# Kernel tuning notes

Measured on AMD Instinct MI355X. Metric: run time of the kernel, lower is better.

Reference implementation:

```python
import jax, jax.numpy as jnp
import numpy as np

HUGE = 1e31  # ops.HUGE_INT
EPS = 1e-20

NUM_ENT, NUM_REL = 100000, 400
ENT_D, REL_D, HIST_D = 256, 256, 512
ACT_D = ENT_D + REL_D          # 512
IN_D = ENT_D + HIST_D + REL_D  # 1024
B, A = 512, 256


def setup_inputs() -> dict:
    key = jax.random.key(0)
    ks = jax.random.split(key, 10)
    s = 0.02
    return {
        "current_entity": jax.random.randint(ks[0], (B,), 0, NUM_ENT),
        "query_relation": jax.random.randint(ks[1], (B,), 0, NUM_REL),
        "encoded_history": jax.random.normal(ks[2], (B, HIST_D), jnp.float32),
        "r_space": jax.random.randint(ks[3], (B, A), 0, NUM_REL),
        "e_space": jax.random.randint(ks[4], (B, A), 0, NUM_ENT),
        "action_mask": jax.random.randint(ks[5], (B, A), 0, 2).astype(jnp.int32),
        "entity_emb": jax.random.normal(ks[6], (NUM_ENT, ENT_D), jnp.float32) * s,
        "relation_emb": jax.random.normal(ks[7], (NUM_REL, REL_D), jnp.float32) * s,
        "W1": jax.random.normal(ks[8], (IN_D, ACT_D), jnp.float32) * s,
        "b1": jnp.zeros((ACT_D,), jnp.float32),
        "W2": jax.random.normal(ks[9], (ACT_D, ACT_D), jnp.float32) * s,
        "b2": jnp.zeros((ACT_D,), jnp.float32),
    }


def reference(current_entity, query_relation, encoded_history, r_space, e_space,
              action_mask, entity_emb, relation_emb, W1, b1, W2, b2):
    # encode_history: [E(cur) | lstm hidden | R(query)] -> [B, IN_D]
    X = jnp.concatenate([entity_emb[current_entity], encoded_history,
                         relation_emb[query_relation]], axis=-1)
    # policy MLP (dropout = identity in eval)
    X2 = jax.nn.relu(X @ W1 + b1) @ W2 + b2          # [B, ACT_D]
    # per-action embeddings: concat(rel, ent) -> [B, A, ACT_D]
    A_emb = jnp.concatenate([relation_emb[r_space], entity_emb[e_space]], axis=-1)
    mask = action_mask.astype(X2.dtype)
    scores = jnp.einsum('bad,bd->ba', A_emb, X2) - (1.0 - mask) * HUGE
    action_dist = jax.nn.softmax(scores, axis=-1)    # [B, A]
    entropy = -jnp.sum(action_dist * jnp.log(action_dist + EPS), axis=-1)  # [B]
    return action_dist, entropy
```

## Files before the change

kernel.cpp:

```cpp
#include <hip/hip_runtime.h>
#include <hip/hip_bf16.h>

#define ENT_D 256
#define REL_D 256
#define HIST_D 512
#define ACT_DD 512
#define IN_DD 1024
#define BB 512
#define AA 256

typedef short bf16x8 __attribute__((ext_vector_type(8)));
typedef float floatx4 __attribute__((ext_vector_type(4)));

__device__ __forceinline__ unsigned short f2bf(float f) {
    unsigned u = __builtin_bit_cast(unsigned, f);
    return (unsigned short)((u + 0x7fffu + ((u >> 16) & 1u)) >> 16);
}


__global__ __launch_bounds__(256) void pack_kernel(
    const int* __restrict__ cur, const int* __restrict__ qrel,
    const float* __restrict__ hist,
    const float* __restrict__ ent_emb, const float* __restrict__ rel_emb,
    const float* __restrict__ W1, const float* __restrict__ W2,
    unsigned short* __restrict__ W1p, unsigned short* __restrict__ W2p,
    unsigned short* __restrict__ Xp)
{
    const int wid  = blockIdx.x * 4 + (threadIdx.x >> 6);
    const int lane = threadIdx.x & 63;
    const int l15  = lane & 15;
    const int quad = lane >> 4;
    unsigned short v[8];

    if (wid < 1024) {
        const int t = wid, nt = t >> 5, kt = t & 31;
        const int n = nt * 16 + l15, k0 = kt * 32 + quad * 8;
#pragma unroll
        for (int j = 0; j < 8; ++j) v[j] = f2bf(W1[(size_t)(k0 + j) * ACT_DD + n]);
        *(bf16x8*)(W1p + ((size_t)t * 64 + lane) * 8) = *(bf16x8*)v;
    } else if (wid < 1536) {
        const int t = wid - 1024, nt = t >> 4, kt = t & 15;
        const int n = nt * 16 + l15, k0 = kt * 32 + quad * 8;
#pragma unroll
        for (int j = 0; j < 8; ++j) v[j] = f2bf(W2[(size_t)(k0 + j) * ACT_DD + n]);
        *(bf16x8*)(W2p + ((size_t)t * 64 + lane) * 8) = *(bf16x8*)v;
    } else {
        const int t = wid - 1536, mt = t >> 5, kt = t & 31;
        const int m = mt * 16 + l15, k0 = kt * 32 + quad * 8;
        const float* src;
        if (k0 < ENT_D)            src = ent_emb + (size_t)cur[m] * ENT_D + k0;
        else if (k0 < ENT_D + HIST_D) src = hist + (size_t)m * HIST_D + (k0 - ENT_D);
        else                       src = rel_emb + (size_t)qrel[m] * REL_D + (k0 - ENT_D - HIST_D);
        float4 a = *(const float4*)src, b = *(const float4*)(src + 4);
        v[0]=f2bf(a.x); v[1]=f2bf(a.y); v[2]=f2bf(a.z); v[3]=f2bf(a.w);
        v[4]=f2bf(b.x); v[5]=f2bf(b.y); v[6]=f2bf(b.z); v[7]=f2bf(b.w);
        *(bf16x8*)(Xp + ((size_t)t * 64 + lane) * 8) = *(bf16x8*)v;
    }
}

__global__ __launch_bounds__(256) void gemm1_kernel(
    const unsigned short* __restrict__ Xp, const unsigned short* __restrict__ W1p,
    const float* __restrict__ b1, unsigned short* __restrict__ Hp)
{
    __shared__ unsigned short sH[1024];
    const int mt = blockIdx.x, wave = threadIdx.x >> 6, lane = threadIdx.x & 63;
    const int nt = blockIdx.y * 4 + wave;

    const bf16x8* Av = (const bf16x8*)Xp  + (size_t)mt * 32 * 64 + lane;
    const bf16x8* Bv = (const bf16x8*)W1p + (size_t)nt * 32 * 64 + lane;
    floatx4 acc = {0.f, 0.f, 0.f, 0.f};
#pragma unroll 8
    for (int kt = 0; kt < 32; ++kt)
        acc = __builtin_amdgcn_mfma_f32_16x16x32_bf16(Av[kt * 64], Bv[kt * 64], acc, 0, 0, 0);

    const int col  = nt * 16 + (lane & 15);
    const float bj = b1[col];
    const int n_loc = wave * 16 + (lane & 15);
    const int tile_loc = n_loc >> 5, quad2 = (n_loc & 31) >> 3, j2 = n_loc & 7;
#pragma unroll
    for (int reg = 0; reg < 4; ++reg) {
        const int row = (lane >> 4) * 4 + reg;
        const float h = fmaxf(acc[reg] + bj, 0.f);
        sH[tile_loc * 512 + (row + 16 * quad2) * 8 + j2] = f2bf(h);
    }
    __syncthreads();
    const int h = threadIdx.x * 4;
    const int tl = h >> 9, rest = h & 511;
    const size_t dst = ((size_t)(mt * 16 + blockIdx.y * 2 + tl) * 512 + rest);
    *(uint2*)(Hp + dst) = *(const uint2*)(sH + h);
}

__global__ __launch_bounds__(256) void gemm2_kernel(
    const unsigned short* __restrict__ Hp, const unsigned short* __restrict__ W2p,
    const float* __restrict__ b2, float* __restrict__ X2)
{
    const int mt = blockIdx.x, wave = threadIdx.x >> 6, lane = threadIdx.x & 63;
    const int nt = blockIdx.y * 4 + wave;

    const bf16x8* Av = (const bf16x8*)Hp  + (size_t)mt * 16 * 64 + lane;
    const bf16x8* Bv = (const bf16x8*)W2p + (size_t)nt * 16 * 64 + lane;
    floatx4 acc = {0.f, 0.f, 0.f, 0.f};
#pragma unroll
    for (int kt = 0; kt < 16; ++kt)
        acc = __builtin_amdgcn_mfma_f32_16x16x32_bf16(Av[kt * 64], Bv[kt * 64], acc, 0, 0, 0);

    const int col = nt * 16 + (lane & 15);
    const float bj = b2[col];
#pragma unroll
    for (int reg = 0; reg < 4; ++reg) {
        const int m = mt * 16 + (lane >> 4) * 4 + reg;
        X2[(size_t)m * ACT_DD + col] = acc[reg] + bj;
    }
}

__global__ __launch_bounds__(512) void score_softmax_kernel(
    const float* __restrict__ X2,
    const int* __restrict__ r_space, const int* __restrict__ e_space,
    const int* __restrict__ amask,
    const float* __restrict__ ent_emb, const float* __restrict__ rel_emb,
    float* __restrict__ dist, float* __restrict__ ent_out)
{
    __shared__ __align__(16) float x2s[ACT_DD];
    __shared__ float sc[AA];
    __shared__ int   list[AA];
    __shared__ int   wcnt[4];
    __shared__ int   n_u_s;
    __shared__ float red[8];

    const int b = blockIdx.x, tid = threadIdx.x;
    const int wave = tid >> 6, lane = tid & 63;

    x2s[tid] = X2[(size_t)b * ACT_DD + tid];

    int m = 0;
    unsigned long long bal = 0;
    int pre = 0;
    if (tid < AA) {
        m = amask[b * AA + tid];
        sc[tid] = 0.0f;
    }
    if (wave < 4) {
        bal = __ballot(m != 0);
        pre = __popcll(bal & ((1ull << lane) - 1ull));
        if (lane == 0) wcnt[wave] = __popcll(bal);
    }
    __syncthreads();

    if (wave < 4) {
        int off = 0;
#pragma unroll
        for (int w = 0; w < 4; ++w) if (w < wave) off += wcnt[w];
        if (m != 0) list[off + pre] = tid;
        if (tid == 0) n_u_s = wcnt[0] + wcnt[1] + wcnt[2] + wcnt[3];
    }
    __syncthreads();

    const int n_u = n_u_s;
    const int padded = (n_u + 63) & ~63;
    if (tid < padded - n_u) list[n_u + tid] = list[0];
    __syncthreads();

    const float4 xr = ((const float4*)&x2s[0])[lane];
    const float4 xe = ((const float4*)&x2s[REL_D])[lane];

    for (int base = wave * 8; base < padded; base += 64) {
        int ai[8], ir[8], ie[8];
#pragma unroll
        for (int i = 0; i < 8; ++i) ai[i] = list[base + i];
#pragma unroll
        for (int i = 0; i < 8; ++i) {
            ir[i] = r_space[b * AA + ai[i]];
            ie[i] = e_space[b * AA + ai[i]];
        }
        float4 r4[8], e4[8];
#pragma unroll
        for (int i = 0; i < 8; ++i)
            r4[i] = ((const float4*)(rel_emb + (size_t)ir[i] * REL_D))[lane];
#pragma unroll
        for (int i = 0; i < 8; ++i)
            e4[i] = ((const float4*)(ent_emb + (size_t)ie[i] * ENT_D))[lane];

        __builtin_amdgcn_sched_barrier(0);

        float p[8];
#pragma unroll
        for (int i = 0; i < 8; ++i)
            p[i] = r4[i].x * xr.x + r4[i].y * xr.y + r4[i].z * xr.z + r4[i].w * xr.w
                 + e4[i].x * xe.x + e4[i].y * xe.y + e4[i].z * xe.z + e4[i].w * xe.w;
#pragma unroll
        for (int off = 32; off > 0; off >>= 1) {
#pragma unroll
            for (int i = 0; i < 8; ++i) p[i] += __shfl_xor(p[i], off, 64);
        }
        if (lane == 0) {
#pragma unroll
            for (int i = 0; i < 8; ++i) sc[ai[i]] = p[i];
        }
    }
    __syncthreads();

    float s = -3.0e38f;
    if (tid < AA) s = (m != 0) ? sc[tid] : (sc[tid] - 1e31f);
    float v = s;
#pragma unroll
    for (int off = 32; off > 0; off >>= 1) v = fmaxf(v, __shfl_xor(v, off, 64));
    if (lane == 0) red[wave] = v;
    __syncthreads();
    float mx = red[0];
#pragma unroll
    for (int w = 1; w < 8; ++w) mx = fmaxf(mx, red[w]);
    __syncthreads();

    const float e = (tid < AA) ? __expf(s - mx) : 0.0f;
    v = e;
#pragma unroll
    for (int off = 32; off > 0; off >>= 1) v += __shfl_xor(v, off, 64);
    if (lane == 0) red[wave] = v;
    __syncthreads();
    float sum = red[0];
#pragma unroll
    for (int w = 1; w < 8; ++w) sum += red[w];
    __syncthreads();

    const float p = e / sum;
    if (tid < AA) dist[(size_t)b * AA + tid] = p;

    v = (tid < AA) ? p * __logf(p + 1e-20f) : 0.0f;
#pragma unroll
    for (int off = 32; off > 0; off >>= 1) v += __shfl_xor(v, off, 64);
    if (lane == 0) red[wave] = v;
    __syncthreads();
    if (tid == 0) {
        float t = red[0];
#pragma unroll
        for (int w = 1; w < 8; ++w) t += red[w];
        ent_out[b] = -t;
    }
}

extern "C" void kernel_launch(void* const* d_in, const int* in_sizes, int n_in,
                              void* d_out, int out_size, void* d_ws, size_t ws_size,
                              hipStream_t stream) {
    const int*   cur      = (const int*)d_in[0];
    const int*   qrel     = (const int*)d_in[1];
    const float* hist     = (const float*)d_in[2];
    const int*   r_space  = (const int*)d_in[3];
    const int*   e_space  = (const int*)d_in[4];
    const int*   amask    = (const int*)d_in[5];
    const float* ent_emb  = (const float*)d_in[6];
    const float* rel_emb  = (const float*)d_in[7];
    const float* W1       = (const float*)d_in[8];
    const float* b1       = (const float*)d_in[9];
    const float* W2       = (const float*)d_in[10];
    const float* b2       = (const float*)d_in[11];

    float* dist    = (float*)d_out;
    float* entropy = dist + (size_t)BB * AA;

    char* w = (char*)d_ws;
    unsigned short* W1p = (unsigned short*)(w);
    unsigned short* W2p = (unsigned short*)(w + (1u << 20));
    unsigned short* Xp  = (unsigned short*)(w + (3u << 19));
    unsigned short* Hp  = (unsigned short*)(w + (5u << 19));
    float*          X2  = (float*)(w + (6u << 19));

    pack_kernel<<<640, 256, 0, stream>>>(cur, qrel, hist, ent_emb, rel_emb, W1, W2, W1p, W2p, Xp);
    gemm1_kernel<<<dim3(32, 8), 256, 0, stream>>>(Xp, W1p, b1, Hp);
    gemm2_kernel<<<dim3(32, 8), 256, 0, stream>>>(Hp, W2p, b2, X2);
    score_softmax_kernel<<<512, 512, 0, stream>>>(X2, r_space, e_space, amask,
                                                  ent_emb, rel_emb, dist, entropy);
}
```

Measured before the change: 180.1 us.

## Fuse bf16 packing of weights and inputs into the GEMM kernels

```diff
diff --git a/kernel.cpp b/kernel.cpp
--- a/kernel.cpp
+++ b/kernel.cpp
@@ -18,98 +18,97 @@
 }
 
 
-__global__ __launch_bounds__(256) void pack_kernel(
+__global__ __launch_bounds__(256) void gemm1_kernel(
     const int* __restrict__ cur, const int* __restrict__ qrel,
     const float* __restrict__ hist,
     const float* __restrict__ ent_emb, const float* __restrict__ rel_emb,
-    const float* __restrict__ W1, const float* __restrict__ W2,
-    unsigned short* __restrict__ W1p, unsigned short* __restrict__ W2p,
-    unsigned short* __restrict__ Xp)
-{
-    const int wid  = blockIdx.x * 4 + (threadIdx.x >> 6);
-    const int lane = threadIdx.x & 63;
-    const int l15  = lane & 15;
-    const int quad = lane >> 4;
-    unsigned short v[8];
-
-    if (wid < 1024) {
-        const int t = wid, nt = t >> 5, kt = t & 31;
-        const int n = nt * 16 + l15, k0 = kt * 32 + quad * 8;
-#pragma unroll
-        for (int j = 0; j < 8; ++j) v[j] = f2bf(W1[(size_t)(k0 + j) * ACT_DD + n]);
-        *(bf16x8*)(W1p + ((size_t)t * 64 + lane) * 8) = *(bf16x8*)v;
-    } else if (wid < 1536) {
-        const int t = wid - 1024, nt = t >> 4, kt = t & 15;
-        const int n = nt * 16 + l15, k0 = kt * 32 + quad * 8;
-#pragma unroll
-        for (int j = 0; j < 8; ++j) v[j] = f2bf(W2[(size_t)(k0 + j) * ACT_DD + n]);
-        *(bf16x8*)(W2p + ((size_t)t * 64 + lane) * 8) = *(bf16x8*)v;
-    } else {
-        const int t = wid - 1536, mt = t >> 5, kt = t & 31;
-        const int m = mt * 16 + l15, k0 = kt * 32 + quad * 8;
-        const float* src;
-        if (k0 < ENT_D)            src = ent_emb + (size_t)cur[m] * ENT_D + k0;
-        else if (k0 < ENT_D + HIST_D) src = hist + (size_t)m * HIST_D + (k0 - ENT_D);
-        else                       src = rel_emb + (size_t)qrel[m] * REL_D + (k0 - ENT_D - HIST_D);
-        float4 a = *(const float4*)src, b = *(const float4*)(src + 4);
-        v[0]=f2bf(a.x); v[1]=f2bf(a.y); v[2]=f2bf(a.z); v[3]=f2bf(a.w);
-        v[4]=f2bf(b.x); v[5]=f2bf(b.y); v[6]=f2bf(b.z); v[7]=f2bf(b.w);
-        *(bf16x8*)(Xp + ((size_t)t * 64 + lane) * 8) = *(bf16x8*)v;
-    }
-}
-
-__global__ __launch_bounds__(256) void gemm1_kernel(
-    const unsigned short* __restrict__ Xp, const unsigned short* __restrict__ W1p,
-    const float* __restrict__ b1, unsigned short* __restrict__ Hp)
+    const float* __restrict__ W1, const float* __restrict__ b1,
+    unsigned short* __restrict__ Hp)
 {
     __shared__ unsigned short sH[1024];
-    const int mt = blockIdx.x, wave = threadIdx.x >> 6, lane = threadIdx.x & 63;
-    const int nt = blockIdx.y * 4 + wave;
-
-    const bf16x8* Av = (const bf16x8*)Xp  + (size_t)mt * 32 * 64 + lane;
-    const bf16x8* Bv = (const bf16x8*)W1p + (size_t)nt * 32 * 64 + lane;
+    const int mt = blockIdx.x, by = blockIdx.y;
+    const int tid = threadIdx.x, w = tid >> 6, lane = tid & 63;
+    const int l15 = lane & 15, quad = lane >> 4;
+    const int nt = by * 4 + w;
+    const int colW = nt * 16 + l15;
+
+    const int m = mt * 16 + l15;
+    const float* rowE = ent_emb + (size_t)cur[m] * ENT_D;
+    const float* rowH = hist + (size_t)m * HIST_D;
+    const float* rowR = rel_emb + (size_t)qrel[m] * REL_D;
+
     floatx4 acc = {0.f, 0.f, 0.f, 0.f};
-#pragma unroll 8
-    for (int kt = 0; kt < 32; ++kt)
-        acc = __builtin_amdgcn_mfma_f32_16x16x32_bf16(Av[kt * 64], Bv[kt * 64], acc, 0, 0, 0);
-
-    const int col  = nt * 16 + (lane & 15);
-    const float bj = b1[col];
-    const int n_loc = wave * 16 + (lane & 15);
+#pragma unroll 4
+    for (int kt = 0; kt < 32; ++kt) {
+        const int k0 = kt * 32 + quad * 8;
+        const float* asrc = (k0 < ENT_D)          ? (rowE + k0)
+                          : (k0 < ENT_D + HIST_D) ? (rowH + (k0 - ENT_D))
+                                                  : (rowR + (k0 - ENT_D - HIST_D));
+        const float4 a0 = ((const float4*)asrc)[0];
+        const float4 a1 = ((const float4*)asrc)[1];
+
+        const float* bsrc = W1 + (size_t)k0 * ACT_DD + colW;
+        float bw[8];
+#pragma unroll
+        for (int j = 0; j < 8; ++j) bw[j] = bsrc[(size_t)j * ACT_DD];
+
+        unsigned short af[8], bf[8];
+        af[0]=f2bf(a0.x); af[1]=f2bf(a0.y); af[2]=f2bf(a0.z); af[3]=f2bf(a0.w);
+        af[4]=f2bf(a1.x); af[5]=f2bf(a1.y); af[6]=f2bf(a1.z); af[7]=f2bf(a1.w);
+#pragma unroll
+        for (int j = 0; j < 8; ++j) bf[j] = f2bf(bw[j]);
+
+        acc = __builtin_amdgcn_mfma_f32_16x16x32_bf16(*(bf16x8*)af, *(bf16x8*)bf, acc, 0, 0, 0);
+    }
+
+    const float bj = b1[colW];
+    const int n_loc = w * 16 + l15;
     const int tile_loc = n_loc >> 5, quad2 = (n_loc & 31) >> 3, j2 = n_loc & 7;
 #pragma unroll
     for (int reg = 0; reg < 4; ++reg) {
-        const int row = (lane >> 4) * 4 + reg;
+        const int row = quad * 4 + reg;
         const float h = fmaxf(acc[reg] + bj, 0.f);
         sH[tile_loc * 512 + (row + 16 * quad2) * 8 + j2] = f2bf(h);
     }
     __syncthreads();
-    const int h = threadIdx.x * 4;
+    const int h = tid * 4;
     const int tl = h >> 9, rest = h & 511;
-    const size_t dst = ((size_t)(mt * 16 + blockIdx.y * 2 + tl) * 512 + rest);
+    const size_t dst = ((size_t)(mt * 16 + by * 2 + tl) * 512 + rest);
     *(uint2*)(Hp + dst) = *(const uint2*)(sH + h);
 }
 
 __global__ __launch_bounds__(256) void gemm2_kernel(
-    const unsigned short* __restrict__ Hp, const unsigned short* __restrict__ W2p,
+    const unsigned short* __restrict__ Hp, const float* __restrict__ W2,
     const float* __restrict__ b2, float* __restrict__ X2)
 {
-    const int mt = blockIdx.x, wave = threadIdx.x >> 6, lane = threadIdx.x & 63;
-    const int nt = blockIdx.y * 4 + wave;
-
-    const bf16x8* Av = (const bf16x8*)Hp  + (size_t)mt * 16 * 64 + lane;
-    const bf16x8* Bv = (const bf16x8*)W2p + (size_t)nt * 16 * 64 + lane;
+    const int mt = blockIdx.x, by = blockIdx.y;
+    const int tid = threadIdx.x, w = tid >> 6, lane = tid & 63;
+    const int l15 = lane & 15, quad = lane >> 4;
+    const int nt = by * 4 + w;
+    const int colW = nt * 16 + l15;
+
+    const bf16x8* Av = (const bf16x8*)Hp + (size_t)mt * 16 * 64 + lane;
+
     floatx4 acc = {0.f, 0.f, 0.f, 0.f};
-#pragma unroll
-    for (int kt = 0; kt < 16; ++kt)
-        acc = __builtin_amdgcn_mfma_f32_16x16x32_bf16(Av[kt * 64], Bv[kt * 64], acc, 0, 0, 0);
-
-    const int col = nt * 16 + (lane & 15);
-    const float bj = b2[col];
+#pragma unroll 4
+    for (int kt = 0; kt < 16; ++kt) {
+        const bf16x8 a = Av[kt * 64];
+        const int k0 = kt * 32 + quad * 8;
+        const float* bsrc = W2 + (size_t)k0 * ACT_DD + colW;
+        float bw[8];
+#pragma unroll
+        for (int j = 0; j < 8; ++j) bw[j] = bsrc[(size_t)j * ACT_DD];
+        unsigned short bf[8];
+#pragma unroll
+        for (int j = 0; j < 8; ++j) bf[j] = f2bf(bw[j]);
+        acc = __builtin_amdgcn_mfma_f32_16x16x32_bf16(a, *(bf16x8*)bf, acc, 0, 0, 0);
+    }
+
+    const float bj = b2[colW];
 #pragma unroll
     for (int reg = 0; reg < 4; ++reg) {
-        const int m = mt * 16 + (lane >> 4) * 4 + reg;
-        X2[(size_t)m * ACT_DD + col] = acc[reg] + bj;
+        const int mm = mt * 16 + quad * 4 + reg;
+        X2[(size_t)mm * ACT_DD + colW] = acc[reg] + bj;
     }
 }
 
@@ -258,15 +257,11 @@
     float* entropy = dist + (size_t)BB * AA;
 
     char* w = (char*)d_ws;
-    unsigned short* W1p = (unsigned short*)(w);
-    unsigned short* W2p = (unsigned short*)(w + (1u << 20));
-    unsigned short* Xp  = (unsigned short*)(w + (3u << 19));
-    unsigned short* Hp  = (unsigned short*)(w + (5u << 19));
-    float*          X2  = (float*)(w + (6u << 19));
-
-    pack_kernel<<<640, 256, 0, stream>>>(cur, qrel, hist, ent_emb, rel_emb, W1, W2, W1p, W2p, Xp);
-    gemm1_kernel<<<dim3(32, 8), 256, 0, stream>>>(Xp, W1p, b1, Hp);
-    gemm2_kernel<<<dim3(32, 8), 256, 0, stream>>>(Hp, W2p, b2, X2);
+    unsigned short* Hp = (unsigned short*)(w);
+    float*          X2 = (float*)(w + (1u << 19));
+
+    gemm1_kernel<<<dim3(32, 8), 256, 0, stream>>>(cur, qrel, hist, ent_emb, rel_emb, W1, b1, Hp);
+    gemm2_kernel<<<dim3(32, 8), 256, 0, stream>>>(Hp, W2, b2, X2);
     score_softmax_kernel<<<512, 512, 0, stream>>>(X2, r_space, e_space, amask,
                                                   ent_emb, rel_emb, dist, entropy);
 }
```

Result: slower. 204.7 us (+13.7%).
